# Optimization experiments

Hardware: AMD Instinct MI355X
Metric: run time of the kernel (lower is better)

Reference implementation:

```python
import jax, jax.numpy as jnp
import numpy as np

BN_EPS = 1e-5
NEG_SLOPE = 0.01  # F.leaky_relu default
MASK_VAL = 1e8


def setup_inputs() -> dict:
    key = jax.random.key(0)
    k1, k2, k3, k4 = jax.random.split(key, 4)
    B, H, D, L = 8, 128, 512, 128
    out_dim, inner = 128, 3 * 128  # inner_dim = (order*support_len + 1) * c_in = 3*H
    x = jax.random.normal(k1, (B, H, D, L), dtype=jnp.float32)
    d_x = jax.random.normal(k2, (B, H, D, L - 1), dtype=jnp.float32)
    conv_w = jax.random.normal(k3, (out_dim, inner), dtype=jnp.float32) * 0.05
    conv_b = jax.random.normal(k4, (out_dim,), dtype=jnp.float32) * 0.05
    bn_gamma = jnp.ones((out_dim,), dtype=jnp.float32)
    bn_beta = jnp.zeros((out_dim,), dtype=jnp.float32)
    return {"x": x, "d_x": d_x, "conv_w": conv_w, "conv_b": conv_b,
            "bn_gamma": bn_gamma, "bn_beta": bn_beta, "max_len": L}


def reference(x, d_x, conv_w, conv_b, bn_gamma, bn_beta, max_len):
    B, H, D, L = x.shape
    V = 2 * D  # node dimension of the pooled graph

    # --- gather-based index pooling ---
    idx = jnp.argmax(jnp.abs(d_x), axis=-1, keepdims=True)        # [B,H,D,1]
    pool_idx = jnp.concatenate([idx, idx + 1], axis=-1)           # [B,H,D,2]
    pv = jnp.take_along_axis(x, pool_idx, axis=-1)                # [B,H,D,2]
    pv = pv.reshape(B, H, V)                                      # [B,H,2D]

    # --- masked-softmax adjacency ---
    adj = jnp.einsum('bhv,bhw->bvw', pv, pv) / V                  # [B,2D,2D]
    eye = jnp.eye(V, dtype=x.dtype)
    adj_masked = adj - eye * MASK_VAL
    pooling_adj = jax.nn.softmax(jax.nn.leaky_relu(adj_masked, NEG_SLOPE), axis=-1) + eye

    # --- GCN: order-2 nconv message passing + 1x1 conv + batchnorm (training stats) ---
    x0 = pv                                                       # [B,H,V] (L=1 squeezed)
    x1 = jnp.einsum('bcv,bvw->bcw', x0, pooling_adj)
    x2 = jnp.einsum('bcv,bvw->bcw', x1, pooling_adj)
    h = jnp.concatenate([x0, x1, x2], axis=1)                     # [B,3H,V]
    h = jnp.einsum('biv,oi->bov', h, conv_w) + conv_b[None, :, None]  # [B,H,V]

    mean = jnp.mean(h, axis=(0, 2), keepdims=True)
    var = jnp.var(h, axis=(0, 2), keepdims=True)
    h = bn_gamma[None, :, None] * (h - mean) * jax.lax.rsqrt(var + BN_EPS) + bn_beta[None, :, None]
    # dropout: identity at inference

    # --- output reshuffle: [B,H,2D] -> [B,2H,D] ---
    res = h.reshape(B, H, D, 2)
    res = jnp.transpose(res, (0, 2, 3, 1))                        # [B,D,2,H]
    res = res.reshape(B, D, 2 * H)
    return jnp.swapaxes(res, -1, -2)                              # [B,2H,D]
```

## Files before the change

### kernel.cpp

```cpp
#include <hip/hip_runtime.h>
#include <cstdint>

#define L_ 128

using bf16   = __bf16;
using bf16x2 = __attribute__((ext_vector_type(2))) __bf16;
using bf16x4 = __attribute__((ext_vector_type(4))) __bf16;
using bf16x8 = __attribute__((ext_vector_type(8))) __bf16;
using f32x4  = __attribute__((ext_vector_type(4))) float;

#define MFMA_B16(a, b, c) __builtin_amdgcn_mfma_f32_16x16x32_bf16((a), (b), (c), 0, 0, 0)

__global__ __launch_bounds__(256) void k_pool(const float* __restrict__ x,
                                              const float* __restrict__ dx,
                                              bf16* __restrict__ pvb) {
  __shared__ float lds[256][33];
  const int tid = threadIdx.x;
  const int64_t rowbase = (int64_t)blockIdx.x * 256;
  const float* dblk = dx + rowbase * 127;

  float bv = -1.0f;
  int bi = 0;

#pragma unroll
  for (int c0 = 0; c0 < 127; c0 += 32) {
    const int tw = (c0 == 96) ? 31 : 32;
    __syncthreads();
#pragma unroll
    for (int i = 0; i < 32; ++i) {
      int e = tid + (i << 8);
      int r = e >> 5;
      int cl = e & 31;
      int c = c0 + cl;
      lds[r][cl] = (c < 127) ? dblk[(int64_t)r * 127 + c] : 0.0f;
    }
    __syncthreads();
    for (int k = 0; k < tw; ++k) {
      float a = fabsf(lds[tid][k]);
      if (a > bv) { bv = a; bi = c0 + k; }
    }
  }

  const int64_t row = rowbase + tid;
  const float* xr = x + row * L_;
  float vx = xr[bi];
  float vy = xr[bi + 1];
  int64_t bh = row >> 9;
  int d = (int)(row & 511);
  bf16x2 o;
  o[0] = (bf16)vx;
  o[1] = (bf16)vy;
  *(bf16x2*)(pvb + (bh << 10) + 2 * d) = o;
}

__global__ __launch_bounds__(256) void k_castw(const float* __restrict__ W,
                                               bf16* __restrict__ Wb) {
  int i = blockIdx.x * 256 + threadIdx.x;
  Wb[i] = (bf16)W[i];
}

__global__ __launch_bounds__(256) void k_tr(const bf16* __restrict__ pvb,
                                            bf16* __restrict__ XT) {
  __shared__ bf16 t[64][66];
  const int b  = blockIdx.x >> 5;
  const int hb = (blockIdx.x >> 4) & 1;
  const int vb = blockIdx.x & 15;
  const int tid = threadIdx.x;
  const bf16* src = pvb + ((int64_t)b << 17) + (int64_t)(hb << 6) * 1024 + (vb << 6);
#pragma unroll
  for (int i = 0; i < 16; ++i) {
    int e = i * 256 + tid;
    int r = e >> 6, c = e & 63;
    t[r][c] = src[(int64_t)r * 1024 + c];
  }
  __syncthreads();
  bf16* dst = XT + ((int64_t)b << 10) * 384 + (int64_t)(vb << 6) * 384 + (hb << 6);
#pragma unroll
  for (int i = 0; i < 16; ++i) {
    int e = i * 256 + tid;
    int vr = e >> 6, hc = e & 63;
    dst[(int64_t)vr * 384 + hc] = t[hc][vr];
  }
}

__global__ __launch_bounds__(256) void k_adj(const bf16* __restrict__ XT,
                                             bf16* __restrict__ AT) {
  const int b  = blockIdx.x >> 6;
  const int vb = blockIdx.x & 63;
  const int tid = threadIdx.x, lane = tid & 63, wid = tid >> 6;
  const int g = lane >> 4, rl = lane & 15;
  const bf16* Xb = XT + (int64_t)b * 1024 * 384;

  __shared__ bf16 lsA[16 * 128];
  __shared__ float redmax[16][4];
  __shared__ float redsum[16][4];

  {
    int row = tid >> 4, c8 = tid & 15;
    bf16x8 v = *(const bf16x8*)(Xb + (int64_t)(vb * 16 + row) * 384 + c8 * 8);
    *(bf16x8*)((char*)lsA + row * 256 + ((c8 ^ (row & 7)) << 4)) = v;
  }
  __syncthreads();

  bf16x8 af[4];
#pragma unroll
  for (int ks = 0; ks < 4; ++ks)
    af[ks] = *(const bf16x8*)((char*)lsA + rl * 256 + ((((ks << 2) | g) ^ (rl & 7)) << 4));

  f32x4 acc[16];
  f32x4 zero = {0.f, 0.f, 0.f, 0.f};
#pragma unroll
  for (int t = 0; t < 16; ++t) acc[t] = zero;

  const int nbase = wid * 256;
#pragma unroll
  for (int t = 0; t < 16; ++t) {
    const bf16* bp = Xb + (int64_t)(nbase + t * 16 + rl) * 384 + g * 8;
#pragma unroll
    for (int ks = 0; ks < 4; ++ks) {
      bf16x8 bfr = *(const bf16x8*)(bp + ks * 32);
      acc[t] = MFMA_B16(af[ks], bfr, acc[t]);
    }
  }

  const int vg0 = vb * 16 + g * 4;
  float rmax[4] = {-1e30f, -1e30f, -1e30f, -1e30f};
#pragma unroll
  for (int t = 0; t < 16; ++t) {
    int n = nbase + t * 16 + rl;
#pragma unroll
    for (int r = 0; r < 4; ++r) {
      float a = acc[t][r] * (1.0f / 1024.0f);
      if (n == vg0 + r) a -= 1e8f;
      a = (a > 0.f) ? a : 0.01f * a;
      acc[t][r] = a;
      rmax[r] = fmaxf(rmax[r], a);
    }
  }
#pragma unroll
  for (int r = 0; r < 4; ++r)
#pragma unroll
    for (int off = 1; off < 16; off <<= 1)
      rmax[r] = fmaxf(rmax[r], __shfl_xor(rmax[r], off, 64));
  if (rl == 0)
#pragma unroll
    for (int r = 0; r < 4; ++r) redmax[g * 4 + r][wid] = rmax[r];
  __syncthreads();
#pragma unroll
  for (int r = 0; r < 4; ++r)
    rmax[r] = fmaxf(fmaxf(redmax[g * 4 + r][0], redmax[g * 4 + r][1]),
                    fmaxf(redmax[g * 4 + r][2], redmax[g * 4 + r][3]));

  float rsum[4] = {0.f, 0.f, 0.f, 0.f};
#pragma unroll
  for (int t = 0; t < 16; ++t)
#pragma unroll
    for (int r = 0; r < 4; ++r) {
      float e = __expf(acc[t][r] - rmax[r]);
      acc[t][r] = e;
      rsum[r] += e;
    }
#pragma unroll
  for (int r = 0; r < 4; ++r)
#pragma unroll
    for (int off = 1; off < 16; off <<= 1) rsum[r] += __shfl_xor(rsum[r], off, 64);
  if (rl == 0)
#pragma unroll
    for (int r = 0; r < 4; ++r) redsum[g * 4 + r][wid] = rsum[r];
  __syncthreads();
#pragma unroll
  for (int r = 0; r < 4; ++r) {
    float s = redsum[g * 4 + r][0] + redsum[g * 4 + r][1] +
              redsum[g * 4 + r][2] + redsum[g * 4 + r][3];
    rsum[r] = 1.0f / s;
  }

  bf16* ATb = AT + ((int64_t)b << 20);
#pragma unroll
  for (int t = 0; t < 16; ++t) {
    int n = nbase + t * 16 + rl;
    bf16x4 o;
#pragma unroll
    for (int r = 0; r < 4; ++r) {
      float v = acc[t][r] * rsum[r] + ((n == vg0 + r) ? 1.0f : 0.0f);
      o[r] = (bf16)v;
    }
    *(bf16x4*)(ATb + (int64_t)n * 1024 + vb * 16 + g * 4) = o;
  }
}

template <int WRITE_ROW, int TCOL>
__global__ __launch_bounds__(256) void k_gemm(const bf16* __restrict__ Xa,
                                              const bf16* __restrict__ AT,
                                              bf16* __restrict__ Yrow,
                                              bf16* __restrict__ XT) {
  const int b  = blockIdx.x >> 4;
  const int n0 = (blockIdx.x & 15) << 6;
  const int tid = threadIdx.x, lane = tid & 63, wid = tid >> 6;
  const int g = lane >> 4, rl = lane & 15;
  const bf16* Xb = Xa + ((int64_t)b << 17);
  const bf16* Ab = AT + ((int64_t)b << 20);

  __shared__ bf16 lsA[128 * 64];
  __shared__ bf16 lsB[64 * 64];

  bf16x8 stA[4], stB[2];

  auto LOAD = [&](int ks) {
    const int k0 = ks << 6;
#pragma unroll
    for (int i = 0; i < 4; ++i) {
      int f = i * 256 + tid;
      int row = f >> 3, c8 = f & 7;
      stA[i] = *(const bf16x8*)(Xb + (int64_t)row * 1024 + k0 + c8 * 8);
    }
#pragma unroll
    for (int i = 0; i < 2; ++i) {
      int f = i * 256 + tid;
      int row = f >> 3, c8 = f & 7;
      stB[i] = *(const bf16x8*)(Ab + (int64_t)(n0 + row) * 1024 + k0 + c8 * 8);
    }
  };
  auto WRITE = [&]() {
#pragma unroll
    for (int i = 0; i < 4; ++i) {
      int f = i * 256 + tid;
      int row = f >> 3, c8 = f & 7;
      *(bf16x8*)((char*)lsA + row * 128 + ((c8 ^ (row & 7)) << 4)) = stA[i];
    }
#pragma unroll
    for (int i = 0; i < 2; ++i) {
      int f = i * 256 + tid;
      int row = f >> 3, c8 = f & 7;
      *(bf16x8*)((char*)lsB + row * 128 + ((c8 ^ (row & 7)) << 4)) = stB[i];
    }
  };

  f32x4 acc[2][4];
  f32x4 zero = {0.f, 0.f, 0.f, 0.f};
#pragma unroll
  for (int mi = 0; mi < 2; ++mi)
#pragma unroll
    for (int ni = 0; ni < 4; ++ni) acc[mi][ni] = zero;

  LOAD(0);
  WRITE();
  __syncthreads();

  for (int ks = 0; ks < 16; ++ks) {
    bf16x8 afr[2][2], bfr[4][2];
#pragma unroll
    for (int mi = 0; mi < 2; ++mi)
#pragma unroll
      for (int ku = 0; ku < 2; ++ku) {
        int row = wid * 32 + mi * 16 + rl;
        afr[mi][ku] = *(const bf16x8*)((char*)lsA + row * 128 +
                                       ((((ku << 2) | g) ^ (rl & 7)) << 4));
      }
#pragma unroll
    for (int ni = 0; ni < 4; ++ni)
#pragma unroll
      for (int ku = 0; ku < 2; ++ku) {
        int row = ni * 16 + rl;
        bfr[ni][ku] = *(const bf16x8*)((char*)lsB + row * 128 +
                                       ((((ku << 2) | g) ^ (rl & 7)) << 4));
      }
    if (ks < 15) LOAD(ks + 1);
    __syncthreads();
    if (ks < 15) WRITE();
#pragma unroll
    for (int ku = 0; ku < 2; ++ku)
#pragma unroll
      for (int mi = 0; mi < 2; ++mi)
#pragma unroll
        for (int ni = 0; ni < 4; ++ni)
          acc[mi][ni] = MFMA_B16(afr[mi][ku], bfr[ni][ku], acc[mi][ni]);
    __syncthreads();
  }

#pragma unroll
  for (int mi = 0; mi < 2; ++mi)
#pragma unroll
    for (int ni = 0; ni < 4; ++ni) {
      int c0 = wid * 32 + mi * 16 + g * 4;
      int w  = n0 + ni * 16 + rl;
      if (WRITE_ROW) {
#pragma unroll
        for (int q = 0; q < 4; ++q)
          Yrow[((int64_t)b << 17) + (int64_t)(c0 + q) * 1024 + w] = (bf16)acc[mi][ni][q];
      }
      bf16x4 o;
#pragma unroll
      for (int q = 0; q < 4; ++q) o[q] = (bf16)acc[mi][ni][q];
      *(bf16x4*)(XT + ((int64_t)b * 1024 + w) * 384 + TCOL + c0) = o;
    }
}

__global__ __launch_bounds__(256) void k_conv(const bf16* __restrict__ Wb,
                                              const bf16* __restrict__ XT,
                                              const float* __restrict__ bias,
                                              float* __restrict__ h) {
  const int b  = blockIdx.x >> 4;
  const int n0 = (blockIdx.x & 15) << 6;
  const int tid = threadIdx.x, lane = tid & 63, wid = tid >> 6;
  const int g = lane >> 4, rl = lane & 15;
  const bf16* Xb = XT + (int64_t)b * 1024 * 384;

  __shared__ bf16 lsA[128 * 64];
  __shared__ bf16 lsB[64 * 64];

  bf16x8 stA[4], stB[2];

  auto LOAD = [&](int ks) {
    const int k0 = ks << 6;
#pragma unroll
    for (int i = 0; i < 4; ++i) {
      int f = i * 256 + tid;
      int row = f >> 3, c8 = f & 7;
      stA[i] = *(const bf16x8*)(Wb + (int64_t)row * 384 + k0 + c8 * 8);
    }
#pragma unroll
    for (int i = 0; i < 2; ++i) {
      int f = i * 256 + tid;
      int row = f >> 3, c8 = f & 7;
      stB[i] = *(const bf16x8*)(Xb + (int64_t)(n0 + row) * 384 + k0 + c8 * 8);
    }
  };
  auto WRITE = [&]() {
#pragma unroll
    for (int i = 0; i < 4; ++i) {
      int f = i * 256 + tid;
      int row = f >> 3, c8 = f & 7;
      *(bf16x8*)((char*)lsA + row * 128 + ((c8 ^ (row & 7)) << 4)) = stA[i];
    }
#pragma unroll
    for (int i = 0; i < 2; ++i) {
      int f = i * 256 + tid;
      int row = f >> 3, c8 = f & 7;
      *(bf16x8*)((char*)lsB + row * 128 + ((c8 ^ (row & 7)) << 4)) = stB[i];
    }
  };

  f32x4 acc[2][4];
  f32x4 zero = {0.f, 0.f, 0.f, 0.f};
#pragma unroll
  for (int mi = 0; mi < 2; ++mi)
#pragma unroll
    for (int ni = 0; ni < 4; ++ni) acc[mi][ni] = zero;

  LOAD(0);
  WRITE();
  __syncthreads();

  for (int ks = 0; ks < 6; ++ks) {
    bf16x8 afr[2][2], bfr[4][2];
#pragma unroll
    for (int mi = 0; mi < 2; ++mi)
#pragma unroll
      for (int ku = 0; ku < 2; ++ku) {
        int row = wid * 32 + mi * 16 + rl;
        afr[mi][ku] = *(const bf16x8*)((char*)lsA + row * 128 +
                                       ((((ku << 2) | g) ^ (rl & 7)) << 4));
      }
#pragma unroll
    for (int ni = 0; ni < 4; ++ni)
#pragma unroll
      for (int ku = 0; ku < 2; ++ku) {
        int row = ni * 16 + rl;
        bfr[ni][ku] = *(const bf16x8*)((char*)lsB + row * 128 +
                                       ((((ku << 2) | g) ^ (rl & 7)) << 4));
      }
    if (ks < 5) LOAD(ks + 1);
    __syncthreads();
    if (ks < 5) WRITE();
#pragma unroll
    for (int ku = 0; ku < 2; ++ku)
#pragma unroll
      for (int mi = 0; mi < 2; ++mi)
#pragma unroll
        for (int ni = 0; ni < 4; ++ni)
          acc[mi][ni] = MFMA_B16(afr[mi][ku], bfr[ni][ku], acc[mi][ni]);
    __syncthreads();
  }

#pragma unroll
  for (int mi = 0; mi < 2; ++mi)
#pragma unroll
    for (int ni = 0; ni < 4; ++ni) {
      int c0 = wid * 32 + mi * 16 + g * 4;
      int w  = n0 + ni * 16 + rl;
#pragma unroll
      for (int q = 0; q < 4; ++q)
        h[((int64_t)(b * 128 + c0 + q) << 10) + w] = acc[mi][ni][q] + bias[c0 + q];
    }
}

__global__ __launch_bounds__(256) void k_stats(const float* __restrict__ hpre,
                                               const float* __restrict__ gamma,
                                               const float* __restrict__ beta,
                                               float2* __restrict__ ss) {
  const int o = blockIdx.x;
  const int tid = threadIdx.x;
  float s = 0.f, s2 = 0.f;
  for (int e = tid; e < 8192; e += 256) {
    int bb = e >> 10, v = e & 1023;
    float val = hpre[((int64_t)(bb * 128 + o) << 10) + v];
    s += val;
    s2 = fmaf(val, val, s2);
  }
#pragma unroll
  for (int off = 1; off < 64; off <<= 1) {
    s  += __shfl_xor(s, off, 64);
    s2 += __shfl_xor(s2, off, 64);
  }
  __shared__ float rs[4], rs2[4];
  int lane = tid & 63, wid = tid >> 6;
  if (lane == 0) { rs[wid] = s; rs2[wid] = s2; }
  __syncthreads();
  if (tid == 0) {
    float S  = rs[0] + rs[1] + rs[2] + rs[3];
    float S2 = rs2[0] + rs2[1] + rs2[2] + rs2[3];
    float mean = S * (1.0f / 8192.0f);
    float var  = S2 * (1.0f / 8192.0f) - mean * mean;
    float istd = rsqrtf(var + 1e-5f);
    float scale = gamma[o] * istd;
    ss[o] = make_float2(scale, beta[o] - mean * scale);
  }
}

__global__ __launch_bounds__(256) void k_out(const float* __restrict__ hpre,
                                             const float2* __restrict__ ss,
                                             float* __restrict__ out) {
  int64_t idx = (int64_t)blockIdx.x * 256 + threadIdx.x;
  int d  = (int)(idx & 511);
  int ph = (int)((idx >> 9) & 255);
  int b  = (int)(idx >> 17);
  int p = ph >> 7, h = ph & 127;
  float2 sc = ss[h];
  float val = hpre[(((int64_t)b * 128 + h) << 10) + 2 * d + p];
  out[idx] = fmaf(val, sc.x, sc.y);
}

extern "C" void kernel_launch(void* const* d_in, const int* in_sizes, int n_in,
                              void* d_out, int out_size, void* d_ws, size_t ws_size,
                              hipStream_t stream) {
  const float* x     = (const float*)d_in[0];
  const float* dx    = (const float*)d_in[1];
  const float* W     = (const float*)d_in[2];
  const float* cb    = (const float*)d_in[3];
  const float* gamma = (const float*)d_in[4];
  const float* beta  = (const float*)d_in[5];

  char* ws = (char*)d_ws;
  bf16*   XcatT = (bf16*)(ws);
  bf16*   AT    = (bf16*)(ws + 6291456);
  bf16*   pvb   = (bf16*)(ws + 23068672);
  bf16*   x1b   = (bf16*)(ws + 25165824);
  bf16*   Wb    = (bf16*)(ws + 27262976);
  float*  h     = (float*)(ws + 27361280);
  float2* ssb   = (float2*)(ws + 31555584);
  float* out    = (float*)d_out;

  k_pool<<<2048, 256, 0, stream>>>(x, dx, pvb);
  k_castw<<<192, 256, 0, stream>>>(W, Wb);
  k_tr<<<256, 256, 0, stream>>>(pvb, XcatT);
  k_adj<<<512, 256, 0, stream>>>(XcatT, AT);
  k_gemm<1, 128><<<128, 256, 0, stream>>>(pvb, AT, x1b, XcatT);
  k_gemm<0, 256><<<128, 256, 0, stream>>>(x1b, AT, nullptr, XcatT);
  k_conv<<<128, 256, 0, stream>>>(Wb, XcatT, cb, h);
  k_stats<<<128, 256, 0, stream>>>(h, gamma, beta, ssb);
  k_out<<<4096, 256, 0, stream>>>(h, ssb, out);
}
```

Before: 169.3 us.

## Use 4 threads per row for argmax pooling and fuse weight cast into conv

```diff
diff --git a/kernel.cpp b/kernel.cpp
--- a/kernel.cpp
+++ b/kernel.cpp
@@ -14,49 +14,36 @@
 __global__ __launch_bounds__(256) void k_pool(const float* __restrict__ x,
                                               const float* __restrict__ dx,
                                               bf16* __restrict__ pvb) {
-  __shared__ float lds[256][33];
-  const int tid = threadIdx.x;
-  const int64_t rowbase = (int64_t)blockIdx.x * 256;
-  const float* dblk = dx + rowbase * 127;
+  const int64_t gt = (int64_t)blockIdx.x * 256 + threadIdx.x;
+  const int64_t row = gt >> 2;
+  const int j = (int)(gt & 3);
+  const float* rp = dx + row * 127;
 
   float bv = -1.0f;
   int bi = 0;
-
-#pragma unroll
-  for (int c0 = 0; c0 < 127; c0 += 32) {
-    const int tw = (c0 == 96) ? 31 : 32;
-    __syncthreads();
-#pragma unroll
-    for (int i = 0; i < 32; ++i) {
-      int e = tid + (i << 8);
-      int r = e >> 5;
-      int cl = e & 31;
-      int c = c0 + cl;
-      lds[r][cl] = (c < 127) ? dblk[(int64_t)r * 127 + c] : 0.0f;
-    }
-    __syncthreads();
-    for (int k = 0; k < tw; ++k) {
-      float a = fabsf(lds[tid][k]);
-      if (a > bv) { bv = a; bi = c0 + k; }
-    }
-  }
-
-  const int64_t row = rowbase + tid;
-  const float* xr = x + row * L_;
-  float vx = xr[bi];
-  float vy = xr[bi + 1];
-  int64_t bh = row >> 9;
-  int d = (int)(row & 511);
-  bf16x2 o;
-  o[0] = (bf16)vx;
-  o[1] = (bf16)vy;
-  *(bf16x2*)(pvb + (bh << 10) + 2 * d) = o;
-}
-
-__global__ __launch_bounds__(256) void k_castw(const float* __restrict__ W,
-                                               bf16* __restrict__ Wb) {
-  int i = blockIdx.x * 256 + threadIdx.x;
-  Wb[i] = (bf16)W[i];
+#pragma unroll
+  for (int i = 0; i < 32; ++i) {
+    int col = 4 * i + j;
+    if (col < 127) {
+      float a = fabsf(rp[col]);
+      if (a > bv) { bv = a; bi = col; }
+    }
+  }
+#pragma unroll
+  for (int off = 1; off <= 2; off <<= 1) {
+    float ov = __shfl_xor(bv, off, 64);
+    int   oi = __shfl_xor(bi, off, 64);
+    if (ov > bv || (ov == bv && oi < bi)) { bv = ov; bi = oi; }
+  }
+  if (j == 0) {
+    const float* xr = x + row * L_;
+    bf16x2 o;
+    o[0] = (bf16)xr[bi];
+    o[1] = (bf16)xr[bi + 1];
+    int64_t bh = row >> 9;
+    int d = (int)(row & 511);
+    *(bf16x2*)(pvb + (bh << 10) + 2 * d) = o;
+  }
 }
 
 __global__ __launch_bounds__(256) void k_tr(const bf16* __restrict__ pvb,
@@ -296,7 +283,7 @@
     }
 }
 
-__global__ __launch_bounds__(256) void k_conv(const bf16* __restrict__ Wb,
+__global__ __launch_bounds__(256) void k_conv(const float* __restrict__ W,
                                               const bf16* __restrict__ XT,
                                               const float* __restrict__ bias,
                                               float* __restrict__ h) {
@@ -317,7 +304,13 @@
     for (int i = 0; i < 4; ++i) {
       int f = i * 256 + tid;
       int row = f >> 3, c8 = f & 7;
-      stA[i] = *(const bf16x8*)(Wb + (int64_t)row * 384 + k0 + c8 * 8);
+      const float* wp = W + (int64_t)row * 384 + k0 + c8 * 8;
+      float4 a0 = *(const float4*)(wp);
+      float4 a1 = *(const float4*)(wp + 4);
+      bf16x8 r;
+      r[0] = (bf16)a0.x; r[1] = (bf16)a0.y; r[2] = (bf16)a0.z; r[3] = (bf16)a0.w;
+      r[4] = (bf16)a1.x; r[5] = (bf16)a1.y; r[6] = (bf16)a1.z; r[7] = (bf16)a1.w;
+      stA[i] = r;
     }
 #pragma unroll
     for (int i = 0; i < 2; ++i) {
@@ -456,18 +449,16 @@
   bf16*   AT    = (bf16*)(ws + 6291456);
   bf16*   pvb   = (bf16*)(ws + 23068672);
   bf16*   x1b   = (bf16*)(ws + 25165824);
-  bf16*   Wb    = (bf16*)(ws + 27262976);
   float*  h     = (float*)(ws + 27361280);
   float2* ssb   = (float2*)(ws + 31555584);
   float* out    = (float*)d_out;
 
-  k_pool<<<2048, 256, 0, stream>>>(x, dx, pvb);
-  k_castw<<<192, 256, 0, stream>>>(W, Wb);
+  k_pool<<<8192, 256, 0, stream>>>(x, dx, pvb);
   k_tr<<<256, 256, 0, stream>>>(pvb, XcatT);
   k_adj<<<512, 256, 0, stream>>>(XcatT, AT);
   k_gemm<1, 128><<<128, 256, 0, stream>>>(pvb, AT, x1b, XcatT);
   k_gemm<0, 256><<<128, 256, 0, stream>>>(x1b, AT, nullptr, XcatT);
-  k_conv<<<128, 256, 0, stream>>>(Wb, XcatT, cb, h);
+  k_conv<<<128, 256, 0, stream>>>(W, XcatT, cb, h);
   k_stats<<<128, 256, 0, stream>>>(h, gamma, beta, ssb);
   k_out<<<4096, 256, 0, stream>>>(h, ssb, out);
 }
```

Measured after the change: 148.6 us. 1.14x faster.
